# Optimization experiments

Hardware: AMD Instinct MI355X
Metric: run time of the kernel (lower is better)

Reference implementation:

```python
import jax, jax.numpy as jnp
import numpy as np

EPS = 1e-06

def rmsnorm(x, w):
    x32 = x.astype(jnp.float32)
    var = jnp.mean(x32 * x32, axis=-1, keepdims=True)
    return w * (x32 * jax.lax.rsqrt(var + EPS)).astype(x.dtype)

def setup_inputs() -> dict:
    B, T, C = 16, 256, 16
    token_dim, text_dim = 1024, 512
    key = jax.random.key(0)
    ks = jax.random.split(key, 8)
    token_embeds = jax.random.normal(ks[0], (B, T, token_dim), dtype=jnp.float32)
    char_embeds = jax.random.normal(ks[1], (B, T, C, text_dim), dtype=jnp.float32)
    filler_embed = jax.random.normal(ks[2], (text_dim,), dtype=jnp.float32)
    mask = jax.random.randint(ks[3], (B, T, C), 0, 2).astype(bool)
    mask = mask.at[0].set(True)  # force max valid count == T*C (static output shape)
    token_ids_mask = jnp.ones((B, T), dtype=bool)
    # xavier-uniform-ish weights
    def xav(k, fan_out, fan_in, gain=1.0):
        lim = gain * np.sqrt(6.0 / (fan_in + fan_out))
        return jax.random.uniform(k, (fan_out, fan_in), jnp.float32, -lim, lim)
    W_down = xav(ks[4], text_dim, token_dim)
    W_proj = xav(ks[5], 3, text_dim, gain=0.2)
    W_fusion = xav(ks[6], text_dim, text_dim)
    w_pre = jnp.ones((token_dim,), jnp.float32)
    w_tok = jnp.ones((text_dim,), jnp.float32)
    w_char = jnp.ones((text_dim,), jnp.float32)
    return {"token_embeds": token_embeds, "token_ids_mask": token_ids_mask,
            "char_embeds": char_embeds, "char_ids_mask": mask,
            "filler_embed": filler_embed, "w_pre": w_pre, "w_tok": w_tok,
            "w_char": w_char, "W_down": W_down, "W_proj": W_proj,
            "W_fusion": W_fusion, "max_valid_chars": T * C}

def reference(token_embeds, token_ids_mask, char_embeds, char_ids_mask,
              filler_embed, w_pre, w_tok, w_char, W_down, W_proj, W_fusion,
              max_valid_chars):
    B, T, C, d = char_embeds.shape
    MV = int(max_valid_chars)
    tok = rmsnorm(token_embeds, w_pre)                       # [B,T,token_dim]
    feats = rmsnorm(jnp.einsum('btk,dk->btd', tok, W_down), w_tok)  # [B,T,d]
    params = jnp.einsum('btd,pd->btp', jax.nn.silu(feats), W_proj)  # [B,T,3]
    scale = params[..., 0][:, :, None, None]                 # [B,T,1,1]
    shift = params[..., 1][:, :, None, None]
    gate = jax.nn.sigmoid(params[..., 2][:, :, None, None])
    cn = rmsnorm(char_embeds, w_char)                        # [B,T,C,d]
    fused = jnp.einsum('btcd,ed->btce', jax.nn.silu(cn * (1.0 + scale) + shift), W_fusion)
    fused = gate * fused + (1.0 - gate) * cn                 # [B,T,C,d]
    flat = fused.reshape(B, T * C, d)
    m = char_ids_mask.reshape(B, T * C).astype(jnp.int32)
    pos = jnp.cumsum(m, axis=1) - 1                          # dest within row
    offs = jnp.arange(B, dtype=jnp.int32)[:, None] * MV
    idx = jnp.where(m > 0, offs + pos, B * MV)               # invalid -> dump slot
    buf = jnp.broadcast_to(filler_embed, (B * MV + 1, d))
    buf = buf.at[idx.reshape(-1)].set(flat.reshape(-1, d))
    return buf[: B * MV].reshape(B, MV, d)
```

## Files before the change

kernel.cpp:

```cpp
#include <hip/hip_runtime.h>
#include <cstdint>
#include <cstddef>

#define EPS 1e-6f

typedef short bf16x8 __attribute__((ext_vector_type(8)));
typedef float f32x4  __attribute__((ext_vector_type(4)));

__device__ __forceinline__ short f2bf(float x) {
    uint32_t u = __builtin_bit_cast(uint32_t, x);
    return (short)((u + 0x7FFFu + ((u >> 16) & 1u)) >> 16);
}

__global__ __launch_bounds__(256) void k_front(
    const void* __restrict__ maskp, int* __restrict__ v_list, int* __restrict__ counts,
    const float* __restrict__ Wf, short* __restrict__ Wfbf,
    const float* __restrict__ Wd, short* __restrict__ Wdbf,
    const float* __restrict__ tokens, const float* __restrict__ w_pre,
    short* __restrict__ tokbf) {
    const int blk = blockIdx.x, tid = threadIdx.x;
    if (blk < 16) {
        __shared__ int wtot[4], woff[4];
        __shared__ int mode_s;
        const int b = blk, lane = tid & 63, wave = tid >> 6;
        if (tid == 0) mode_s = 0;
        __syncthreads();
        {
            int bad = 0;
#pragma unroll
            for (int q = 0; q < 4; ++q)
                bad |= (((const uint32_t*)maskp)[q * 256 + tid] > 1u) ? 1 : 0;
            if (bad) mode_s = 1;
        }
        __syncthreads();
        int f[16];
        if (mode_s) {
            const uint4 v = ((const uint4*)maskp)[(b << 8) + tid];
            const uint32_t ws[4] = {v.x, v.y, v.z, v.w};
#pragma unroll
            for (int q = 0; q < 4; ++q) {
                f[q * 4 + 0] = (ws[q] & 0x000000ffu) != 0;
                f[q * 4 + 1] = (ws[q] & 0x0000ff00u) != 0;
                f[q * 4 + 2] = (ws[q] & 0x00ff0000u) != 0;
                f[q * 4 + 3] = (ws[q] & 0xff000000u) != 0;
            }
        } else {
            const uint4* mp = (const uint4*)maskp + ((size_t)b << 10) + tid * 4;
#pragma unroll
            for (int q = 0; q < 4; ++q) {
                const uint4 v = mp[q];
                f[q * 4 + 0] = v.x != 0; f[q * 4 + 1] = v.y != 0;
                f[q * 4 + 2] = v.z != 0; f[q * 4 + 3] = v.w != 0;
            }
        }
        int c = 0;
#pragma unroll
        for (int q = 0; q < 16; ++q) c += f[q];
        int incl = c;
#pragma unroll
        for (int off = 1; off < 64; off <<= 1) {
            const int n = __shfl_up(incl, off);
            if (lane >= off) incl += n;
        }
        if (lane == 63) wtot[wave] = incl;
        __syncthreads();
        if (tid == 0) {
            int run = 0;
#pragma unroll
            for (int wv = 0; wv < 4; ++wv) { woff[wv] = run; run += wtot[wv]; }
            counts[b] = run;
        }
        __syncthreads();
        int base = woff[wave] + incl - c;
        int* vl = v_list + (b << 12);
        const int i0 = tid * 16;
#pragma unroll
        for (int q = 0; q < 16; ++q)
            if (f[q]) vl[base++] = i0 + q;
    } else if (blk < 784) {
        const int gid = (blk - 16) * 256 + tid;
        const float* s; short* d; int i;
        if (gid < 65536) { s = Wf; d = Wfbf; i = gid; }
        else             { s = Wd; d = Wdbf; i = gid - 65536; }
        const float4 v = ((const float4*)s)[i];
        short4 o;
        o.x = f2bf(v.x); o.y = f2bf(v.y); o.z = f2bf(v.z); o.w = f2bf(v.w);
        ((short4*)d)[i] = o;
    } else {
        const int lane = tid & 63, wave = tid >> 6;
        const int row = (blk - 784) * 4 + wave;
        const float* xp = tokens + (size_t)row * 1024 + lane * 16;
        float4 x[4];
#pragma unroll
        for (int q = 0; q < 4; ++q) x[q] = *(const float4*)&xp[q * 4];
        float ss = 0.f;
#pragma unroll
        for (int q = 0; q < 4; ++q)
            ss += x[q].x * x[q].x + x[q].y * x[q].y + x[q].z * x[q].z + x[q].w * x[q].w;
#pragma unroll
        for (int off = 32; off > 0; off >>= 1) ss += __shfl_down(ss, off);
        ss = __shfl(ss, 0);
        const float r = rsqrtf(ss * (1.0f / 1024.0f) + EPS);
        const float* wp = w_pre + lane * 16;
        short* op = tokbf + (size_t)row * 1024 + lane * 16;
#pragma unroll
        for (int h = 0; h < 2; ++h) {
            bf16x8 o;
#pragma unroll
            for (int q = 0; q < 2; ++q) {
                const float4 wv = *(const float4*)&wp[h * 8 + q * 4];
                const float4 xv = x[h * 2 + q];
                o[q * 4 + 0] = f2bf(xv.x * wv.x * r);
                o[q * 4 + 1] = f2bf(xv.y * wv.y * r);
                o[q * 4 + 2] = f2bf(xv.z * wv.z * r);
                o[q * 4 + 3] = f2bf(xv.w * wv.w * r);
            }
            *(bf16x8*)&op[h * 8] = o;
        }
    }
}

__global__ __launch_bounds__(256) void k_gemm_tok(const short* __restrict__ tokbf,
                                                  const short* __restrict__ Wdbf,
                                                  float* __restrict__ feats) {
    __shared__ short As[2][128 * 32];
    __shared__ short Bs[2][128 * 32];
    const int tid = threadIdx.x, lane = tid & 63, w = tid >> 6;
    const int kt = blockIdx.x >> 7;
    const int mt = (blockIdx.x >> 2) & 31, nt = blockIdx.x & 3;
    const int wm = w >> 1, wn = w & 1;
    const int kbase = kt * 512;
    const short* hA = tokbf + (size_t)mt * 128 * 1024;
    const short* wB = Wdbf + (size_t)nt * 128 * 1024;

    f32x4 acc[4][4];
#pragma unroll
    for (int mi = 0; mi < 4; ++mi)
#pragma unroll
        for (int ni = 0; ni < 4; ++ni) acc[mi][ni] = (f32x4)0.f;

    const int rA = lane & 15, ch = lane >> 4;

    auto STAGE = [&](int bufi, int kk) {
#pragma unroll
        for (int q = 0; q < 2; ++q) {
            const int cid = (w * 2 + q) * 64 + lane;
            const int r = cid >> 2, kc = cid & 3;
            const int kcs = kc ^ ((r >> 1) & 3);
            const size_t go = (size_t)r * 1024 + kk + kcs * 8;
            __builtin_amdgcn_global_load_lds(
                (const __attribute__((address_space(1))) uint32_t*)(hA + go),
                (__attribute__((address_space(3))) uint32_t*)&As[bufi][(w * 2 + q) * 512], 16, 0, 0);
            __builtin_amdgcn_global_load_lds(
                (const __attribute__((address_space(1))) uint32_t*)(wB + go),
                (__attribute__((address_space(3))) uint32_t*)&Bs[bufi][(w * 2 + q) * 512], 16, 0, 0);
        }
    };
    auto COMPUTE = [&](int bufi) {
        bf16x8 af[4], bfr[4];
#pragma unroll
        for (int mi = 0; mi < 4; ++mi) {
            const int row = wm * 64 + mi * 16 + rA;
            af[mi] = *(const bf16x8*)&As[bufi][row * 32 + ((ch ^ ((row >> 1) & 3)) << 3)];
        }
#pragma unroll
        for (int ni = 0; ni < 4; ++ni) {
            const int row = wn * 64 + ni * 16 + rA;
            bfr[ni] = *(const bf16x8*)&Bs[bufi][row * 32 + ((ch ^ ((row >> 1) & 3)) << 3)];
        }
#pragma unroll
        for (int mi = 0; mi < 4; ++mi)
#pragma unroll
            for (int ni = 0; ni < 4; ++ni)
                acc[mi][ni] = __builtin_amdgcn_mfma_f32_16x16x32_bf16(af[mi], bfr[ni], acc[mi][ni], 0, 0, 0);
    };

    STAGE(0, kbase);
    STAGE(1, kbase + 32);
    __syncthreads();
#pragma unroll
    for (int t = 0; t < 16; ++t) {
        if (t >= 2) {
            if (t < 15) asm volatile("s_waitcnt vmcnt(4)" ::: "memory");
            else        asm volatile("s_waitcnt vmcnt(0)" ::: "memory");
            __builtin_amdgcn_sched_barrier(0);
        }
        __builtin_amdgcn_s_barrier();
        COMPUTE(t & 1);
        __builtin_amdgcn_s_barrier();
        if (t < 14) STAGE(t & 1, kbase + (t + 2) * 32);
    }

    float* fo = feats + (size_t)kt * 4096 * 512;
    const int rowb = mt * 128 + wm * 64 + (lane >> 4) * 4;
    const int colb = nt * 128 + wn * 64 + (lane & 15);
#pragma unroll
    for (int mi = 0; mi < 4; ++mi)
#pragma unroll
        for (int ni = 0; ni < 4; ++ni)
#pragma unroll
            for (int rg = 0; rg < 4; ++rg)
                fo[(size_t)(rowb + mi * 16 + rg) * 512 + colb + ni * 16] = acc[mi][ni][rg];
}

__global__ __launch_bounds__(256) void k_params(
    const float* __restrict__ feats_pre, const float* __restrict__ w_tok,
    const float* __restrict__ W_proj, float* __restrict__ params) {
    const int tk = blockIdx.x * 4 + (threadIdx.x >> 6);
    const int lane = threadIdx.x & 63;
    const int d0 = lane * 8;
    const float* fp0 = feats_pre + (size_t)tk * 512 + d0;
    const float* fp1 = fp0 + (size_t)4096 * 512;
    const float4 a0 = *(const float4*)&fp0[0];
    const float4 a1 = *(const float4*)&fp0[4];
    const float4 b0 = *(const float4*)&fp1[0];
    const float4 b1 = *(const float4*)&fp1[4];
    const float4 f0 = make_float4(a0.x + b0.x, a0.y + b0.y, a0.z + b0.z, a0.w + b0.w);
    const float4 f1 = make_float4(a1.x + b1.x, a1.y + b1.y, a1.z + b1.z, a1.w + b1.w);
    float ss = f0.x * f0.x + f0.y * f0.y + f0.z * f0.z + f0.w * f0.w
             + f1.x * f1.x + f1.y * f1.y + f1.z * f1.z + f1.w * f1.w;
#pragma unroll
    for (int off = 32; off > 0; off >>= 1) ss += __shfl_down(ss, off);
    ss = __shfl(ss, 0);
    const float rms = rsqrtf(ss * (1.0f / 512.0f) + EPS);

    const float4 wt0 = *(const float4*)&w_tok[d0];
    const float4 wt1 = *(const float4*)&w_tok[d0 + 4];
    float fv[8] = {f0.x, f0.y, f0.z, f0.w, f1.x, f1.y, f1.z, f1.w};
    float wv[8] = {wt0.x, wt0.y, wt0.z, wt0.w, wt1.x, wt1.y, wt1.z, wt1.w};
    float s[8];
#pragma unroll
    for (int j = 0; j < 8; ++j) {
        const float v = fv[j] * wv[j] * rms;
        s[j] = v / (1.0f + expf(-v));
    }
    float p[3];
#pragma unroll
    for (int q = 0; q < 3; ++q) {
        const float* Wp = W_proj + (size_t)q * 512 + d0;
        const float4 a = *(const float4*)&Wp[0];
        const float4 c = *(const float4*)&Wp[4];
        p[q] = s[0] * a.x + s[1] * a.y + s[2] * a.z + s[3] * a.w
             + s[4] * c.x + s[5] * c.y + s[6] * c.z + s[7] * c.w;
#pragma unroll
        for (int off = 32; off > 0; off >>= 1) p[q] += __shfl_down(p[q], off);
    }
    if (lane == 0) {
        float* po = params + (size_t)tk * 4;
        po[0] = 1.0f + p[0];
        po[1] = p[1];
        po[2] = 1.0f / (1.0f + expf(-p[2]));
        po[3] = 0.f;
    }
}

__global__ __launch_bounds__(256) void k_prep(
    const float* __restrict__ chars, const float* __restrict__ w_char,
    const float* __restrict__ params, const int* __restrict__ v_list,
    const int* __restrict__ counts, short* __restrict__ hb,
    float* __restrict__ rms_l, float* __restrict__ g_l) {
    const int tid = threadIdx.x, lane = tid & 63, wave = tid >> 6;
    const int b = blockIdx.x >> 10;
    const int j = (blockIdx.x & 1023) * 4 + wave;
    const int cnt = counts[b];
    const int cpad = (cnt + 127) & ~127;
    if (j >= cpad) return;
    short* hrow = hb + ((size_t)(b << 12) + j) * 512 + lane * 8;
    if (j >= cnt) {
        *(bf16x8*)hrow = (bf16x8)0;
        return;
    }
    const int i = v_list[(b << 12) + j];
    const float* xp = chars + ((size_t)(b << 12) + i) * 512 + lane * 8;
    const float4 x0 = *(const float4*)&xp[0];
    const float4 x1 = *(const float4*)&xp[4];
    float ss = x0.x * x0.x + x0.y * x0.y + x0.z * x0.z + x0.w * x0.w
             + x1.x * x1.x + x1.y * x1.y + x1.z * x1.z + x1.w * x1.w;
#pragma unroll
    for (int off = 32; off > 0; off >>= 1) ss += __shfl_down(ss, off);
    ss = __shfl(ss, 0);
    const float rms = rsqrtf(ss * (1.0f / 512.0f) + EPS);
    const float* pp = params + (size_t)((b << 8) + (i >> 4)) * 4;
    const float s1 = pp[0], sh = pp[1], g = pp[2];
    const float4 w0 = *(const float4*)&w_char[lane * 8];
    const float4 w1 = *(const float4*)&w_char[lane * 8 + 4];
    float xv[8] = {x0.x, x0.y, x0.z, x0.w, x1.x, x1.y, x1.z, x1.w};
    float wv[8] = {w0.x, w0.y, w0.z, w0.w, w1.x, w1.y, w1.z, w1.w};
    bf16x8 o;
#pragma unroll
    for (int q = 0; q < 8; ++q) {
        const float cn = wv[q] * xv[q] * rms;
        const float a = cn * s1 + sh;
        o[q] = f2bf(a / (1.0f + expf(-a)));
    }
    *(bf16x8*)hrow = o;
    if (lane == 0) {
        rms_l[(b << 12) + j] = rms;
        g_l[(b << 12) + j] = g;
    }
}

__global__ __launch_bounds__(256) void k_gemm_fus(
    const short* __restrict__ hb, const short* __restrict__ Wbf,
    const float* __restrict__ chars, const float* __restrict__ w_char,
    const float* __restrict__ rms_l, const float* __restrict__ g_l,
    const int* __restrict__ v_list, const int* __restrict__ counts,
    const float* __restrict__ filler, float* __restrict__ out) {
    const int wg = (blockIdx.x & 7) * 256 + (blockIdx.x >> 3);
    const int b = wg >> 7;
    const int mt = (wg >> 2) & 31;
    const int nt = wg & 3;
    const int tid = threadIdx.x, lane = tid & 63, w = tid >> 6;
    const int cnt = counts[b];
    const int row0 = mt * 128;
    if (row0 >= cnt) {
        const int colb0 = nt * 128;
        const float4 f = *(const float4*)(filler + colb0 + (tid & 31) * 4);
        float* o0 = out + ((size_t)(b << 12) + row0) * 512 + colb0 + (tid & 31) * 4;
        for (int r = tid >> 5; r < 128; r += 8)
            *(float4*)&o0[(size_t)r * 512] = f;
        return;
    }

    __shared__ short As[2][128 * 32];
    __shared__ short Bs[2][128 * 32];
    __shared__ float g_s[128], rms_s[128];
    __shared__ int idx_s[128];
    const int wm = w >> 1, wn = w & 1;

    const short* hA = hb + ((size_t)(b << 12) + row0) * 512;
    const short* wB = Wbf + (size_t)nt * 128 * 512;

    f32x4 acc[4][4];
#pragma unroll
    for (int mi = 0; mi < 4; ++mi)
#pragma unroll
        for (int ni = 0; ni < 4; ++ni) acc[mi][ni] = (f32x4)0.f;

    const int rA = lane & 15, ch = lane >> 4;

    auto STAGE = [&](int bufi, int kk) {
#pragma unroll
        for (int q = 0; q < 2; ++q) {
            const int cid = (w * 2 + q) * 64 + lane;
            const int r = cid >> 2, kc = cid & 3;
            const int kcs = kc ^ ((r >> 1) & 3);
            const size_t go = (size_t)r * 512 + kk + kcs * 8;
            __builtin_amdgcn_global_load_lds(
                (const __attribute__((address_space(1))) uint32_t*)(hA + go),
                (__attribute__((address_space(3))) uint32_t*)&As[bufi][(w * 2 + q) * 512], 16, 0, 0);
            __builtin_amdgcn_global_load_lds(
                (const __attribute__((address_space(1))) uint32_t*)(wB + go),
                (__attribute__((address_space(3))) uint32_t*)&Bs[bufi][(w * 2 + q) * 512], 16, 0, 0);
        }
    };
    auto COMPUTE = [&](int bufi) {
        bf16x8 af[4], bfr[4];
#pragma unroll
        for (int mi = 0; mi < 4; ++mi) {
            const int row = wm * 64 + mi * 16 + rA;
            af[mi] = *(const bf16x8*)&As[bufi][row * 32 + ((ch ^ ((row >> 1) & 3)) << 3)];
        }
#pragma unroll
        for (int ni = 0; ni < 4; ++ni) {
            const int row = wn * 64 + ni * 16 + rA;
            bfr[ni] = *(const bf16x8*)&Bs[bufi][row * 32 + ((ch ^ ((row >> 1) & 3)) << 3)];
        }
#pragma unroll
        for (int mi = 0; mi < 4; ++mi)
#pragma unroll
            for (int ni = 0; ni < 4; ++ni)
                acc[mi][ni] = __builtin_amdgcn_mfma_f32_16x16x32_bf16(af[mi], bfr[ni], acc[mi][ni], 0, 0, 0);
    };

    STAGE(0, 0);
    STAGE(1, 32);
    if (tid < 128) {
        const int j = row0 + tid;
        const bool valid = j < cnt;
        idx_s[tid] = valid ? v_list[(b << 12) + j] : 0;
        g_s[tid]   = valid ? g_l[(b << 12) + j] : 0.f;
        rms_s[tid] = valid ? rms_l[(b << 12) + j] : 0.f;
    }
    __syncthreads();
#pragma unroll
    for (int t = 0; t < 16; ++t) {
        if (t >= 2) {
            if (t < 15) asm volatile("s_waitcnt vmcnt(4)" ::: "memory");
            else        asm volatile("s_waitcnt vmcnt(0)" ::: "memory");
            __builtin_amdgcn_sched_barrier(0);
        }
        __builtin_amdgcn_s_barrier();
        COMPUTE(t & 1);
        __builtin_amdgcn_s_barrier();
        if (t < 14) STAGE(t & 1, (t + 2) * 32);
    }

    const int colb = nt * 128 + wn * 64 + (lane & 15);
    float wcv[4];
#pragma unroll
    for (int ni = 0; ni < 4; ++ni) wcv[ni] = w_char[colb + ni * 16];
#pragma unroll
    for (int mi = 0; mi < 4; ++mi) {
#pragma unroll
        for (int rg = 0; rg < 4; ++rg) {
            const int jl = wm * 64 + mi * 16 + (lane >> 4) * 4 + rg;
            const int j = row0 + jl;
            const size_t orow = ((size_t)(b << 12) + j) * 512;
            if (j < cnt) {
                const float g = g_s[jl], rm = rms_s[jl];
                const size_t xrow = ((size_t)(b << 12) + idx_s[jl]) * 512;
#pragma unroll
                for (int ni = 0; ni < 4; ++ni) {
                    const int col = colb + ni * 16;
                    const float x = chars[xrow + col];
                    const float cn = wcv[ni] * x * rm;
                    out[orow + col] = g * acc[mi][ni][rg] + (1.0f - g) * cn;
                }
            } else {
#pragma unroll
                for (int ni = 0; ni < 4; ++ni) {
                    const int col = colb + ni * 16;
                    out[orow + col] = filler[col];
                }
            }
        }
    }
}

extern "C" void kernel_launch(void* const* d_in, const int* in_sizes, int n_in,
                              void* d_out, int out_size, void* d_ws, size_t ws_size,
                              hipStream_t stream) {
    const float* tokens = (const float*)d_in[0];
    const float* chars  = (const float*)d_in[2];
    const void*  cmask  = d_in[3];
    const float* filler = (const float*)d_in[4];
    const float* w_pre  = (const float*)d_in[5];
    const float* w_tok  = (const float*)d_in[6];
    const float* w_char = (const float*)d_in[7];
    const float* W_down = (const float*)d_in[8];
    const float* W_proj = (const float*)d_in[9];
    const float* W_fus  = (const float*)d_in[10];
    float* out = (float*)d_out;

    float* feats_pre = (float*)d_ws;
    float* params    = feats_pre + (size_t)2 * 4096 * 512;
    int*   counts    = (int*)(params + (size_t)4096 * 4);
    int*   v_list    = counts + 16;
    float* rms_l     = (float*)(v_list + 65536);
    float* g_l       = rms_l + 65536;
    short* Wbf       = (short*)(g_l + 65536);
    short* hb        = Wbf + (size_t)512 * 512;
    short* tokbf     = hb + (size_t)16 * 4096 * 512;
    short* Wdbf      = tokbf + (size_t)4096 * 1024;

    k_front<<<1808, 256, 0, stream>>>(cmask, v_list, counts, W_fus, Wbf,
                                      W_down, Wdbf, tokens, w_pre, tokbf);
    k_gemm_tok<<<256, 256, 0, stream>>>(tokbf, Wdbf, feats_pre);
    k_params<<<1024, 256, 0, stream>>>(feats_pre, w_tok, W_proj, params);
    k_prep<<<16384, 256, 0, stream>>>(chars, w_char, params, v_list, counts, hb, rms_l, g_l);
    k_gemm_fus<<<2048, 256, 0, stream>>>(hb, Wbf, chars, w_char, rms_l, g_l,
                                         v_list, counts, filler, out);
}
```

Before: 337.5 us.

## Fuse char prep into fusion GEMM, computing bf16 A operand on the fly

Removes the separate k_prep kernel and its bf16 hb intermediate. The fusion GEMM now gathers char rows itself, computes each row's RMS, applies norm, modulation and SiLU in registers, and writes bf16 A tiles into LDS. Tiles change to 64 rows by the full 512 output columns with 512 threads, so every A row is prepared exactly once per block. This drops the round-trip through global memory for the intermediate. The cost is an extra pass over chars for the RMS, SiLU work on the GEMM's critical path, larger LDS for B and fewer blocks.

New measurement: 367.7 us. 1.09x slower.

```diff
diff --git a/kernel.cpp b/kernel.cpp
--- a/kernel.cpp
+++ b/kernel.cpp
@@ -5,7 +5,11 @@
 #define EPS 1e-6f
 
 typedef short bf16x8 __attribute__((ext_vector_type(8)));
+typedef short bf16x4 __attribute__((ext_vector_type(4)));
 typedef float f32x4  __attribute__((ext_vector_type(4)));
+
+#define AS1 __attribute__((address_space(1)))
+#define AS3 __attribute__((address_space(3)))
 
 __device__ __forceinline__ short f2bf(float x) {
     uint32_t u = __builtin_bit_cast(uint32_t, x);
@@ -149,11 +153,11 @@
             const int kcs = kc ^ ((r >> 1) & 3);
             const size_t go = (size_t)r * 1024 + kk + kcs * 8;
             __builtin_amdgcn_global_load_lds(
-                (const __attribute__((address_space(1))) uint32_t*)(hA + go),
-                (__attribute__((address_space(3))) uint32_t*)&As[bufi][(w * 2 + q) * 512], 16, 0, 0);
+                (const AS1 uint32_t*)(hA + go),
+                (AS3 uint32_t*)&As[bufi][(w * 2 + q) * 512], 16, 0, 0);
             __builtin_amdgcn_global_load_lds(
-                (const __attribute__((address_space(1))) uint32_t*)(wB + go),
-                (__attribute__((address_space(3))) uint32_t*)&Bs[bufi][(w * 2 + q) * 512], 16, 0, 0);
+                (const AS1 uint32_t*)(wB + go),
+                (AS3 uint32_t*)&Bs[bufi][(w * 2 + q) * 512], 16, 0, 0);
         }
     };
     auto COMPUTE = [&](int bufi) {
@@ -254,176 +258,147 @@
     }
 }
 
-__global__ __launch_bounds__(256) void k_prep(
-    const float* __restrict__ chars, const float* __restrict__ w_char,
-    const float* __restrict__ params, const int* __restrict__ v_list,
-    const int* __restrict__ counts, short* __restrict__ hb,
-    float* __restrict__ rms_l, float* __restrict__ g_l) {
-    const int tid = threadIdx.x, lane = tid & 63, wave = tid >> 6;
-    const int b = blockIdx.x >> 10;
-    const int j = (blockIdx.x & 1023) * 4 + wave;
-    const int cnt = counts[b];
-    const int cpad = (cnt + 127) & ~127;
-    if (j >= cpad) return;
-    short* hrow = hb + ((size_t)(b << 12) + j) * 512 + lane * 8;
-    if (j >= cnt) {
-        *(bf16x8*)hrow = (bf16x8)0;
-        return;
-    }
-    const int i = v_list[(b << 12) + j];
-    const float* xp = chars + ((size_t)(b << 12) + i) * 512 + lane * 8;
-    const float4 x0 = *(const float4*)&xp[0];
-    const float4 x1 = *(const float4*)&xp[4];
-    float ss = x0.x * x0.x + x0.y * x0.y + x0.z * x0.z + x0.w * x0.w
-             + x1.x * x1.x + x1.y * x1.y + x1.z * x1.z + x1.w * x1.w;
-#pragma unroll
-    for (int off = 32; off > 0; off >>= 1) ss += __shfl_down(ss, off);
-    ss = __shfl(ss, 0);
-    const float rms = rsqrtf(ss * (1.0f / 512.0f) + EPS);
-    const float* pp = params + (size_t)((b << 8) + (i >> 4)) * 4;
-    const float s1 = pp[0], sh = pp[1], g = pp[2];
-    const float4 w0 = *(const float4*)&w_char[lane * 8];
-    const float4 w1 = *(const float4*)&w_char[lane * 8 + 4];
-    float xv[8] = {x0.x, x0.y, x0.z, x0.w, x1.x, x1.y, x1.z, x1.w};
-    float wv[8] = {w0.x, w0.y, w0.z, w0.w, w1.x, w1.y, w1.z, w1.w};
-    bf16x8 o;
-#pragma unroll
-    for (int q = 0; q < 8; ++q) {
-        const float cn = wv[q] * xv[q] * rms;
-        const float a = cn * s1 + sh;
-        o[q] = f2bf(a / (1.0f + expf(-a)));
-    }
-    *(bf16x8*)hrow = o;
-    if (lane == 0) {
-        rms_l[(b << 12) + j] = rms;
-        g_l[(b << 12) + j] = g;
-    }
-}
-
-__global__ __launch_bounds__(256) void k_gemm_fus(
-    const short* __restrict__ hb, const short* __restrict__ Wbf,
-    const float* __restrict__ chars, const float* __restrict__ w_char,
-    const float* __restrict__ rms_l, const float* __restrict__ g_l,
+__global__ __launch_bounds__(512) void k_gemm_fus(
+    const short* __restrict__ Wbf, const float* __restrict__ chars,
+    const float* __restrict__ w_char, const float* __restrict__ params,
     const int* __restrict__ v_list, const int* __restrict__ counts,
     const float* __restrict__ filler, float* __restrict__ out) {
-    const int wg = (blockIdx.x & 7) * 256 + (blockIdx.x >> 3);
-    const int b = wg >> 7;
-    const int mt = (wg >> 2) & 31;
-    const int nt = wg & 3;
+    const int bid = blockIdx.x;
+    const int b = bid >> 6, mt = bid & 63;
     const int tid = threadIdx.x, lane = tid & 63, w = tid >> 6;
     const int cnt = counts[b];
-    const int row0 = mt * 128;
+    const int row0 = mt * 64;
     if (row0 >= cnt) {
-        const int colb0 = nt * 128;
-        const float4 f = *(const float4*)(filler + colb0 + (tid & 31) * 4);
-        float* o0 = out + ((size_t)(b << 12) + row0) * 512 + colb0 + (tid & 31) * 4;
-        for (int r = tid >> 5; r < 128; r += 8)
+        const int col = (tid & 127) * 4;
+        const float4 f = *(const float4*)&filler[col];
+        float* o0 = out + ((size_t)(b << 12) + row0) * 512 + col;
+#pragma unroll
+        for (int r = tid >> 7; r < 64; r += 4)
             *(float4*)&o0[(size_t)r * 512] = f;
         return;
     }
 
-    __shared__ short As[2][128 * 32];
-    __shared__ short Bs[2][128 * 32];
-    __shared__ float g_s[128], rms_s[128];
-    __shared__ int idx_s[128];
-    const int wm = w >> 1, wn = w & 1;
-
-    const short* hA = hb + ((size_t)(b << 12) + row0) * 512;
-    const short* wB = Wbf + (size_t)nt * 128 * 512;
-
-    f32x4 acc[4][4];
-#pragma unroll
-    for (int mi = 0; mi < 4; ++mi)
-#pragma unroll
-        for (int ni = 0; ni < 4; ++ni) acc[mi][ni] = (f32x4)0.f;
-
-    const int rA = lane & 15, ch = lane >> 4;
-
-    auto STAGE = [&](int bufi, int kk) {
-#pragma unroll
-        for (int q = 0; q < 2; ++q) {
-            const int cid = (w * 2 + q) * 64 + lane;
-            const int r = cid >> 2, kc = cid & 3;
-            const int kcs = kc ^ ((r >> 1) & 3);
-            const size_t go = (size_t)r * 512 + kk + kcs * 8;
-            __builtin_amdgcn_global_load_lds(
-                (const __attribute__((address_space(1))) uint32_t*)(hA + go),
-                (__attribute__((address_space(3))) uint32_t*)&As[bufi][(w * 2 + q) * 512], 16, 0, 0);
-            __builtin_amdgcn_global_load_lds(
-                (const __attribute__((address_space(1))) uint32_t*)(wB + go),
-                (__attribute__((address_space(3))) uint32_t*)&Bs[bufi][(w * 2 + q) * 512], 16, 0, 0);
-        }
-    };
-    auto COMPUTE = [&](int bufi) {
-        bf16x8 af[4], bfr[4];
-#pragma unroll
-        for (int mi = 0; mi < 4; ++mi) {
-            const int row = wm * 64 + mi * 16 + rA;
-            af[mi] = *(const bf16x8*)&As[bufi][row * 32 + ((ch ^ ((row >> 1) & 3)) << 3)];
-        }
-#pragma unroll
-        for (int ni = 0; ni < 4; ++ni) {
-            const int row = wn * 64 + ni * 16 + rA;
-            bfr[ni] = *(const bf16x8*)&Bs[bufi][row * 32 + ((ch ^ ((row >> 1) & 3)) << 3)];
-        }
-#pragma unroll
-        for (int mi = 0; mi < 4; ++mi)
-#pragma unroll
-            for (int ni = 0; ni < 4; ++ni)
-                acc[mi][ni] = __builtin_amdgcn_mfma_f32_16x16x32_bf16(af[mi], bfr[ni], acc[mi][ni], 0, 0, 0);
-    };
-
-    STAGE(0, 0);
-    STAGE(1, 32);
-    if (tid < 128) {
+    __shared__ short As[2][64 * 32];
+    __shared__ short Bs[2][512 * 32];
+    __shared__ float rms_s[64], s1_s[64], sh_s[64], g_s[64];
+    __shared__ int idx_s[64];
+
+    if (tid < 64) {
         const int j = row0 + tid;
         const bool valid = j < cnt;
-        idx_s[tid] = valid ? v_list[(b << 12) + j] : 0;
-        g_s[tid]   = valid ? g_l[(b << 12) + j] : 0.f;
-        rms_s[tid] = valid ? rms_l[(b << 12) + j] : 0.f;
+        const int idx = valid ? v_list[(b << 12) + j] : -1;
+        idx_s[tid] = idx;
+        if (valid) {
+            const float* pp = params + (size_t)((b << 8) + (idx >> 4)) * 4;
+            s1_s[tid] = pp[0]; sh_s[tid] = pp[1]; g_s[tid] = pp[2];
+        } else { s1_s[tid] = 0.f; sh_s[tid] = 0.f; g_s[tid] = 0.f; }
     }
     __syncthreads();
+
+    {
+        const int r = tid >> 3, li = tid & 7;
+        const int id = idx_s[r];
+        float ss = 0.f;
+        if (id >= 0) {
+            const float* rp = chars + (((size_t)(b << 12) + id) << 9) + li * 4;
+#pragma unroll
+            for (int s = 0; s < 16; ++s) {
+                const float4 v = *(const float4*)&rp[s * 32];
+                ss += v.x * v.x + v.y * v.y + v.z * v.z + v.w * v.w;
+            }
+        }
+        ss += __shfl_xor(ss, 1); ss += __shfl_xor(ss, 2); ss += __shfl_xor(ss, 4);
+        if (li == 0) rms_s[r] = rsqrtf(ss * (1.0f / 512.0f) + EPS);
+    }
+    __syncthreads();
+
+    const int ar = tid >> 3;
+    const int ac4 = (tid & 7) * 4;
+    const int aidr = idx_s[ar] < 0 ? 0 : idx_s[ar];
+    const float arms = rms_s[ar], as1 = s1_s[ar], ash = sh_s[ar];
+    const float* arow = chars + (((size_t)(b << 12) + aidr) << 9) + ac4;
+    const int a_sidx = ar * 32 + ((((ac4 >> 3) ^ ((ar >> 1) & 3))) << 3) + (ac4 & 4);
+
+    const int wm = w >> 1, wn = w & 1;
+    const int rA = lane & 15, ch = lane >> 4;
+
+    f32x4 acc[16];
+#pragma unroll
+    for (int i = 0; i < 16; ++i) acc[i] = (f32x4)0.f;
+    f32x4 areg[2];
+
+    auto ALOAD = [&](int t) { areg[t & 1] = *(const f32x4*)&arow[t * 32]; };
+    auto ASTORE = [&](int t) {
+        const float* wc = &w_char[t * 32 + ac4];
+        bf16x4 hv;
+#pragma unroll
+        for (int q = 0; q < 4; ++q) {
+            const float cn = wc[q] * areg[t & 1][q] * arms;
+            const float a = cn * as1 + ash;
+            hv[q] = f2bf(a / (1.0f + expf(-a)));
+        }
+        *(bf16x4*)&As[t & 1][a_sidx] = hv;
+    };
+    auto BSTAGE = [&](int t) {
+        const int kk = t * 32;
+#pragma unroll
+        for (int q = 0; q < 4; ++q) {
+            const int eid = (w * 4 + q) * 16 + (lane >> 2);
+            const int kc = lane & 3;
+            const int kcs = kc ^ ((eid >> 1) & 3);
+            const size_t go = (size_t)eid * 512 + kk + kcs * 8;
+            __builtin_amdgcn_global_load_lds(
+                (const AS1 uint32_t*)(Wbf + go),
+                (AS3 uint32_t*)&Bs[t & 1][(w * 4 + q) * 512], 16, 0, 0);
+        }
+    };
+    auto COMPUTE = [&](int t) {
+        const int arw = wm * 16 + rA;
+        const bf16x8 af = *(const bf16x8*)&As[t & 1][arw * 32 + ((ch ^ ((arw >> 1) & 3)) << 3)];
+#pragma unroll
+        for (int ni = 0; ni < 16; ++ni) {
+            const int e = wn * 256 + ni * 16 + rA;
+            const bf16x8 bfr = *(const bf16x8*)&Bs[t & 1][e * 32 + ((ch ^ ((e >> 1) & 3)) << 3)];
+            acc[ni] = __builtin_amdgcn_mfma_f32_16x16x32_bf16(af, bfr, acc[ni], 0, 0, 0);
+        }
+    };
+
+    ALOAD(0);
+    BSTAGE(0);
 #pragma unroll
     for (int t = 0; t < 16; ++t) {
-        if (t >= 2) {
-            if (t < 15) asm volatile("s_waitcnt vmcnt(4)" ::: "memory");
-            else        asm volatile("s_waitcnt vmcnt(0)" ::: "memory");
-            __builtin_amdgcn_sched_barrier(0);
-        }
+        ASTORE(t);
+        if (t < 15) ALOAD(t + 1);
+        __builtin_amdgcn_sched_barrier(0);
+        if (t < 15) asm volatile("s_waitcnt vmcnt(1)" ::: "memory");
+        else        asm volatile("s_waitcnt vmcnt(0)" ::: "memory");
+        __builtin_amdgcn_sched_barrier(0);
+        asm volatile("s_waitcnt lgkmcnt(0)" ::: "memory");
+        __builtin_amdgcn_sched_barrier(0);
         __builtin_amdgcn_s_barrier();
-        COMPUTE(t & 1);
-        __builtin_amdgcn_s_barrier();
-        if (t < 14) STAGE(t & 1, (t + 2) * 32);
-    }
-
-    const int colb = nt * 128 + wn * 64 + (lane & 15);
-    float wcv[4];
-#pragma unroll
-    for (int ni = 0; ni < 4; ++ni) wcv[ni] = w_char[colb + ni * 16];
-#pragma unroll
-    for (int mi = 0; mi < 4; ++mi) {
-#pragma unroll
-        for (int rg = 0; rg < 4; ++rg) {
-            const int jl = wm * 64 + mi * 16 + (lane >> 4) * 4 + rg;
-            const int j = row0 + jl;
-            const size_t orow = ((size_t)(b << 12) + j) * 512;
-            if (j < cnt) {
-                const float g = g_s[jl], rm = rms_s[jl];
-                const size_t xrow = ((size_t)(b << 12) + idx_s[jl]) * 512;
-#pragma unroll
-                for (int ni = 0; ni < 4; ++ni) {
-                    const int col = colb + ni * 16;
-                    const float x = chars[xrow + col];
-                    const float cn = wcv[ni] * x * rm;
-                    out[orow + col] = g * acc[mi][ni][rg] + (1.0f - g) * cn;
-                }
-            } else {
-#pragma unroll
-                for (int ni = 0; ni < 4; ++ni) {
-                    const int col = colb + ni * 16;
-                    out[orow + col] = filler[col];
-                }
+        if (t < 15) BSTAGE(t + 1);
+        COMPUTE(t);
+    }
+
+    const int cb = wn * 256 + (lane & 15);
+#pragma unroll
+    for (int rg = 0; rg < 4; ++rg) {
+        const int jl = wm * 16 + (lane >> 4) * 4 + rg;
+        const int j = row0 + jl;
+        float* orow = out + ((size_t)(b << 12) + j) * 512 + cb;
+        if (j < cnt) {
+            const float g = g_s[jl], rm = rms_s[jl];
+            const float* xrow = chars + (((size_t)(b << 12) + idx_s[jl]) << 9) + cb;
+#pragma unroll
+            for (int ni = 0; ni < 16; ++ni) {
+                const float x = xrow[ni * 16];
+                const float cn = w_char[cb + ni * 16] * x * rm;
+                orow[ni * 16] = g * acc[ni][rg] + (1.0f - g) * cn;
             }
+        } else {
+#pragma unroll
+            for (int ni = 0; ni < 16; ++ni)
+                orow[ni * 16] = filler[cb + ni * 16];
         }
     }
 }
@@ -447,18 +422,14 @@
     float* params    = feats_pre + (size_t)2 * 4096 * 512;
     int*   counts    = (int*)(params + (size_t)4096 * 4);
     int*   v_list    = counts + 16;
-    float* rms_l     = (float*)(v_list + 65536);
-    float* g_l       = rms_l + 65536;
-    short* Wbf       = (short*)(g_l + 65536);
-    short* hb        = Wbf + (size_t)512 * 512;
-    short* tokbf     = hb + (size_t)16 * 4096 * 512;
+    short* Wbf       = (short*)(v_list + 65536);
+    short* tokbf     = Wbf + (size_t)512 * 512;
     short* Wdbf      = tokbf + (size_t)4096 * 1024;
 
     k_front<<<1808, 256, 0, stream>>>(cmask, v_list, counts, W_fus, Wbf,
                                       W_down, Wdbf, tokens, w_pre, tokbf);
     k_gemm_tok<<<256, 256, 0, stream>>>(tokbf, Wdbf, feats_pre);
     k_params<<<1024, 256, 0, stream>>>(feats_pre, w_tok, W_proj, params);
-    k_prep<<<16384, 256, 0, stream>>>(chars, w_char, params, v_list, counts, hb, rms_l, g_l);
-    k_gemm_fus<<<2048, 256, 0, stream>>>(hb, Wbf, chars, w_char, rms_l, g_l,
+    k_gemm_fus<<<1024, 512, 0, stream>>>(Wbf, chars, w_char, params,
                                          v_list, counts, filler, out);
 }
```
